# Optimization experiments

Measured on AMD Instinct MI355X. Metric: run time of the kernel, lower is better.

Reference implementation:

```python
import jax, jax.numpy as jnp
import numpy as np

N = 50000   # nodes (cells)
E = 800000  # directed edges
D = 512     # input/output feature dim (genes)
H = D // 64 # bottleneck dim = 8
LN_EPS = 1e-5


def setup_inputs() -> dict:
    key = jax.random.key(0)
    ks = jax.random.split(key, 6)
    x = jax.random.normal(ks[0], (N, D), dtype=jnp.float32)
    edge_index = jax.random.randint(ks[1], (2, E), 0, N, dtype=jnp.int64)
    size_factors = jax.random.uniform(ks[2], (N, 1), dtype=jnp.float32) + 0.5
    s1 = float(1.0 / np.sqrt(D))
    W1 = jax.random.uniform(ks[3], (D, H), jnp.float32, -s1, s1)
    b1 = jnp.zeros((H,), jnp.float32)
    gamma = jnp.ones((H,), jnp.float32)
    beta = jnp.zeros((H,), jnp.float32)
    s2 = float(1.0 / np.sqrt(H))
    W2 = jax.random.uniform(ks[4], (H, D), jnp.float32, -s2, s2)
    b2 = jnp.zeros((D,), jnp.float32)
    return {"x": x, "size_factors": size_factors, "W1": W1, "b1": b1,
            "gamma": gamma, "beta": beta, "W2": W2, "b2": b2,
            "edge_index": edge_index}


def _gcn_conv(x, W, b, src, dst, norm):
    # PyG GCNConv: linear transform, then sym-normalized scatter-add aggregation.
    h = x @ W                                   # [N, out]
    msg = h[src] * norm[:, None]                # [E+N, out] gather + scale
    out = jax.ops.segment_sum(msg, dst, num_segments=N)  # scatter-add
    return out + b


def reference(x, size_factors, W1, b1, gamma, beta, W2, b2, edge_index):
    loops = jnp.arange(N, dtype=edge_index.dtype)
    src = jnp.concatenate([edge_index[0], loops])  # add self-loops
    dst = jnp.concatenate([edge_index[1], loops])
    deg = jax.ops.segment_sum(jnp.ones_like(src, dtype=x.dtype), dst,
                              num_segments=N)       # deg >= 1 via self-loops
    dinv = jax.lax.rsqrt(deg)
    norm = dinv[src] * dinv[dst]                    # [E+N]

    h = _gcn_conv(x, W1, b1, src, dst, norm)        # [N, H]
    mu = jnp.mean(h, axis=-1, keepdims=True)
    var = jnp.var(h, axis=-1, keepdims=True)
    h = (h - mu) * jax.lax.rsqrt(var + LN_EPS) * gamma + beta
    h = jax.nn.relu(h)
    # dropout p=0.0 -> identity
    out = jax.nn.relu(_gcn_conv(h, W2, b2, src, dst, norm))  # [N, D]
    return out * size_factors
```

## Files before the change

kernel.cpp:

```cpp
#include <hip/hip_runtime.h>

#define NN 50000
#define EE 800000
#define DD 512
#define HH 8
#define BA 256
#define CHUNK 3125
#define NBIN 391
#define NBH 512
#define BCAP 2432
#define BPAD 2880
#define GBLK 782
#define NTILE 3125
#define AGBLK 1563

typedef short bf16x8 __attribute__((ext_vector_type(8)));
typedef float f32x4 __attribute__((ext_vector_type(4)));

union U16 { uint4 u; bf16x8 v; unsigned short h[8]; };

__device__ __forceinline__ unsigned short f2bf(float f) {
    union { float f; unsigned int i; } c; c.f = f;
    unsigned int i = c.i;
    i += 0x7fffu + ((i >> 16) & 1u);
    return (unsigned short)(i >> 16);
}

__global__ __launch_bounds__(256) void k_gemm1_hist(const float4* __restrict__ x4,
                                                    const float* __restrict__ W1,
                                                    const int* __restrict__ dst,
                                                    float* __restrict__ t1,
                                                    int* __restrict__ blockhist) {
    __shared__ int smem[4096];
    int t = threadIdx.x;
    if (blockIdx.x >= GBLK) {
        int blk = blockIdx.x - GBLK;
        int* h = smem;
        h[t] = 0; h[t + 256] = 0; __syncthreads();
        int base = blk * CHUNK;
#pragma unroll
        for (int it = 0; it < 13; ++it) {
            int i = it * 256 + t;
            if (i < CHUNK) atomicAdd(&h[dst[base + i] >> 7], 1);
        }
        __syncthreads();
        blockhist[blk * NBH + t] = h[t];
        blockhist[blk * NBH + t + 256] = h[t + 256];
        return;
    }
    unsigned short* sbf = (unsigned short*)smem;
    for (int i = t; i < 16 * 64 * 8; i += 256) {
        int lane = (i >> 3) & 63, j = i & 7;
        int n = lane & 15;
        int k = (i >> 9) * 32 + ((lane >> 4) * 8) + j;
        sbf[i] = (n < HH) ? f2bf(W1[k * HH + n]) : (unsigned short)0;
    }
    __syncthreads();
    int wave = t >> 6, lane = t & 63;
    int tile = blockIdx.x * 4 + wave;
    if (tile >= NTILE) return;
    int node0 = tile * 16;
    int m = lane & 15, q = lane >> 4;
    const float4* xrow = x4 + (size_t)(node0 + m) * (DD / 4) + q * 2;
    const uint4* bfrag = (const uint4*)sbf;
    f32x4 acc = {0.f, 0.f, 0.f, 0.f};

    float4 bufA[8], bufB[8];
#define LOADG(buf, g)                                                      \
    _Pragma("unroll")                                                      \
    for (int s = 0; s < 4; ++s) {                                          \
        buf[2 * s]     = xrow[((g) * 4 + s) * 8];                          \
        buf[2 * s + 1] = xrow[((g) * 4 + s) * 8 + 1];                      \
    }
#define MFMAG(buf, g)                                                      \
    _Pragma("unroll")                                                      \
    for (int s = 0; s < 4; ++s) {                                          \
        U16 a, b;                                                          \
        float4 u0 = buf[2 * s], u1 = buf[2 * s + 1];                       \
        a.h[0] = f2bf(u0.x); a.h[1] = f2bf(u0.y);                          \
        a.h[2] = f2bf(u0.z); a.h[3] = f2bf(u0.w);                          \
        a.h[4] = f2bf(u1.x); a.h[5] = f2bf(u1.y);                          \
        a.h[6] = f2bf(u1.z); a.h[7] = f2bf(u1.w);                          \
        b.u = bfrag[((g) * 4 + s) * 64 + lane];                            \
        acc = __builtin_amdgcn_mfma_f32_16x16x32_bf16(a.v, b.v, acc, 0, 0, 0); \
    }
    LOADG(bufA, 0)
    LOADG(bufB, 1)
    MFMAG(bufA, 0)
    LOADG(bufA, 2)
    MFMAG(bufB, 1)
    LOADG(bufB, 3)
    MFMAG(bufA, 2)
    MFMAG(bufB, 3)
#undef LOADG
#undef MFMAG
    if (m < HH) {
        int base = (node0 + q * 4) * HH + m;
        t1[base]          = acc[0];
        t1[base + HH]     = acc[1];
        t1[base + 2 * HH] = acc[2];
        t1[base + 3 * HH] = acc[3];
    }
}

__global__ __launch_bounds__(256) void k_scan_a(int* __restrict__ blockhist,
                                                int* __restrict__ binTotal) {
    __shared__ int s[256];
    int bin = blockIdx.x, t = threadIdx.x;
    int v = blockhist[t * NBH + bin];
    s[t] = v; __syncthreads();
    for (int off = 1; off < 256; off <<= 1) {
        int x = (t >= off) ? s[t - off] : 0;
        __syncthreads();
        if (t >= off) s[t] += x;
        __syncthreads();
    }
    blockhist[t * NBH + bin] = s[t] - v;
    if (t == 255) binTotal[bin] = s[255];
}

__global__ __launch_bounds__(512) void k_scan_b(const int* __restrict__ binTotal,
                                                int* __restrict__ binBase,
                                                float* __restrict__ t1) {
    __shared__ int s[512];
    int t = threadIdx.x;
    int v = (t < NBIN) ? binTotal[t] : 0;
    s[t] = v; __syncthreads();
    for (int off = 1; off < 512; off <<= 1) {
        int x = (t >= off) ? s[t - off] : 0;
        __syncthreads();
        if (t >= off) s[t] += x;
        __syncthreads();
    }
    if (t < NBIN) binBase[t] = s[t] - v;
    if (t == 511) binBase[NBIN] = s[511];
    if (t < HH) t1[(size_t)NN * HH + t] = 0.f;
}

__global__ __launch_bounds__(256) void k_scatter(const int* __restrict__ eidx,
                                                 const int* __restrict__ blockhist,
                                                 const int* __restrict__ binBase,
                                                 int* __restrict__ bucket) {
    __shared__ int cur[NBH];
    int t = threadIdx.x, blk = blockIdx.x;
    cur[t] = (t < NBIN) ? binBase[t] + blockhist[blk * NBH + t] : 0;
    {
        int i = t + 256;
        cur[i] = (i < NBIN) ? binBase[i] + blockhist[blk * NBH + i] : 0;
    }
    __syncthreads();
    int base = blk * CHUNK;
#pragma unroll
    for (int it = 0; it < 13; ++it) {
        int i = it * 256 + t;
        if (i < CHUNK) {
            int s = eidx[base + i], d = eidx[EE + base + i];
            int pos = atomicAdd(&cur[d >> 7], 1);
            bucket[pos] = (s << 7) | (d & 127);
        }
    }
}

__global__ __launch_bounds__(256) void k_build(const int* __restrict__ bucket,
                                               const int* __restrict__ binBase,
                                               int* __restrict__ beg,
                                               int* __restrict__ endp,
                                               int* __restrict__ adj,
                                               float* __restrict__ dinvA,
                                               float* __restrict__ t1) {
    __shared__ int smem[BCAP + BPAD + 384];
    int t = threadIdx.x;
    int bin = blockIdx.x;
    int n0 = bin << 7;
    int segStart = binBase[bin];
    int count = binBase[bin + 1] - segStart;
    if (count > BCAP) count = BCAP;
    int* lds_in  = smem;
    int* lds_out = smem + BCAP;
    int* cnt     = smem + BCAP + BPAD;
    int* off     = smem + BCAP + BPAD + 128;
    int* cur2    = smem + BCAP + BPAD + 256;
    if (t < 128) cnt[t] = 0;
    __syncthreads();
    for (int i = t; i < count; i += 256) {
        int p = bucket[segStart + i];
        lds_in[i] = p;
        atomicAdd(&cnt[p & 127], 1);
    }
    __syncthreads();
    int pcnt = 0;
    if (t < 128) { pcnt = (cnt[t] + 3) & ~3; off[t] = pcnt; }
    __syncthreads();
    for (int o = 1; o < 128; o <<= 1) {
        int x = (t >= o && t < 128) ? off[t - o] : 0;
        __syncthreads();
        if (t >= o && t < 128) off[t] += x;
        __syncthreads();
    }
    int pbase = ((segStart + 3) & ~3) + bin * 512;
    if (t < 128) {
        int pexcl = off[t] - pcnt;
        cur2[t] = pexcl;
        int n = n0 + t;
        if (n < NN) {
            beg[n]  = pbase + pexcl;
            endp[n] = pbase + pexcl + pcnt;
            float dv = rsqrtf((float)cnt[t] + 1.0f);
            dinvA[n] = dv;
            float4* tp = (float4*)(t1 + (size_t)n * HH);
            float4 a = tp[0], b = tp[1];
            a.x *= dv; a.y *= dv; a.z *= dv; a.w *= dv;
            b.x *= dv; b.y *= dv; b.z *= dv; b.w *= dv;
            tp[0] = a; tp[1] = b;
        }
    }
    __syncthreads();
    int paddedCount = off[127];
    for (int i = t; i < paddedCount; i += 256)
        lds_out[i] = NN;
    __syncthreads();
    for (int i = t; i < count; i += 256) {
        int p = lds_in[i];
        int pos = atomicAdd(&cur2[p & 127], 1);
        lds_out[pos] = p >> 7;
    }
    __syncthreads();
    for (int i = t; i < paddedCount; i += 256)
        adj[pbase + i] = lds_out[i];
}

__global__ __launch_bounds__(256) void k_agg1(const float* __restrict__ t1,
                                              const int* __restrict__ beg,
                                              const int* __restrict__ endp,
                                              const float* __restrict__ dinvA,
                                              const float* __restrict__ b1,
                                              const float* __restrict__ gma,
                                              const float* __restrict__ bta,
                                              const int* __restrict__ adj,
                                              float* __restrict__ h2) {
    if (blockIdx.x == 0 && threadIdx.x < HH)
        h2[(size_t)NN * HH + threadIdx.x] = 0.f;
    int gid = blockIdx.x * 256 + threadIdx.x;
    int n = gid >> 3, f = gid & 7;
    if (n >= NN) return;
    int i = beg[n], e = endp[n];
    float dv = dinvA[n];
    float acc = t1[(size_t)n * HH + f];
    const int4* a4 = (const int4*)adj;
    for (; i + 8 <= e; i += 8) {
        int4 e0 = a4[i >> 2], e1 = a4[(i >> 2) + 1];
        float v0 = t1[(size_t)e0.x * HH + f], v1 = t1[(size_t)e0.y * HH + f];
        float v2 = t1[(size_t)e0.z * HH + f], v3 = t1[(size_t)e0.w * HH + f];
        float v4 = t1[(size_t)e1.x * HH + f], v5 = t1[(size_t)e1.y * HH + f];
        float v6 = t1[(size_t)e1.z * HH + f], v7 = t1[(size_t)e1.w * HH + f];
        acc += ((v0 + v1) + (v2 + v3)) + ((v4 + v5) + (v6 + v7));
    }
    if (i < e) {
        int4 e0 = a4[i >> 2];
        float v0 = t1[(size_t)e0.x * HH + f], v1 = t1[(size_t)e0.y * HH + f];
        float v2 = t1[(size_t)e0.z * HH + f], v3 = t1[(size_t)e0.w * HH + f];
        acc += (v0 + v1) + (v2 + v3);
    }
    acc = acc * dv + b1[f];
    float s = acc;
    s += __shfl_xor(s, 1); s += __shfl_xor(s, 2); s += __shfl_xor(s, 4);
    float mu = s * 0.125f;
    float dx = acc - mu;
    float sq = dx * dx;
    sq += __shfl_xor(sq, 1); sq += __shfl_xor(sq, 2); sq += __shfl_xor(sq, 4);
    float rs = rsqrtf(sq * 0.125f + 1e-5f);
    h2[(size_t)n * HH + f] = fmaxf(dx * rs * gma[f] + bta[f], 0.f) * dv;
}

__global__ __launch_bounds__(256) void k_agg2_gemm2(const float* __restrict__ h2,
                                                    const int* __restrict__ beg,
                                                    const int* __restrict__ endp,
                                                    const float* __restrict__ dinvA,
                                                    const float* __restrict__ W2,
                                                    const float* __restrict__ b2,
                                                    const float* __restrict__ sf,
                                                    const int* __restrict__ adj,
                                                    float* __restrict__ out) {
    __shared__ float sA[32 * 8];
    int tid = threadIdx.x;
    int c = tid & 63, g = tid >> 6, d0 = c * 8;
    float w[8][8];
#pragma unroll
    for (int k = 0; k < 8; ++k) {
        float4 u0 = *(const float4*)(W2 + k * DD + d0);
        float4 u1 = *(const float4*)(W2 + k * DD + d0 + 4);
        w[k][0] = u0.x; w[k][1] = u0.y; w[k][2] = u0.z; w[k][3] = u0.w;
        w[k][4] = u1.x; w[k][5] = u1.y; w[k][6] = u1.z; w[k][7] = u1.w;
    }
    float bb[8];
    {
        float4 u0 = *(const float4*)(b2 + d0);
        float4 u1 = *(const float4*)(b2 + d0 + 4);
        bb[0] = u0.x; bb[1] = u0.y; bb[2] = u0.z; bb[3] = u0.w;
        bb[4] = u1.x; bb[5] = u1.y; bb[6] = u1.z; bb[7] = u1.w;
    }
    int nl = tid >> 3, f = tid & 7;
    int n = blockIdx.x * 32 + nl;
    if (n < NN) {
        int i = beg[n], e = endp[n];
        float dv = dinvA[n];
        float acc = h2[(size_t)n * HH + f];
        const int4* a4 = (const int4*)adj;
        for (; i + 8 <= e; i += 8) {
            int4 e0 = a4[i >> 2], e1 = a4[(i >> 2) + 1];
            float v0 = h2[(size_t)e0.x * HH + f], v1 = h2[(size_t)e0.y * HH + f];
            float v2 = h2[(size_t)e0.z * HH + f], v3 = h2[(size_t)e0.w * HH + f];
            float v4 = h2[(size_t)e1.x * HH + f], v5 = h2[(size_t)e1.y * HH + f];
            float v6 = h2[(size_t)e1.z * HH + f], v7 = h2[(size_t)e1.w * HH + f];
            acc += ((v0 + v1) + (v2 + v3)) + ((v4 + v5) + (v6 + v7));
        }
        if (i < e) {
            int4 e0 = a4[i >> 2];
            float v0 = h2[(size_t)e0.x * HH + f], v1 = h2[(size_t)e0.y * HH + f];
            float v2 = h2[(size_t)e0.z * HH + f], v3 = h2[(size_t)e0.w * HH + f];
            acc += (v0 + v1) + (v2 + v3);
        }
        sA[nl * 8 + f] = acc * dv;
    }
    __syncthreads();
#pragma unroll
    for (int i = 0; i < 8; ++i) {
        int rrow = i * 4 + g;
        int n2 = blockIdx.x * 32 + rrow;
        if (n2 < NN) {
            float a[8];
#pragma unroll
            for (int j = 0; j < 8; ++j) a[j] = sA[rrow * 8 + j];
            float s = sf[n2];
            float acc[8];
#pragma unroll
            for (int j = 0; j < 8; ++j) acc[j] = bb[j];
#pragma unroll
            for (int k = 0; k < 8; ++k)
#pragma unroll
                for (int j = 0; j < 8; ++j) acc[j] += a[k] * w[k][j];
            float4 o0 = make_float4(fmaxf(acc[0], 0.f) * s, fmaxf(acc[1], 0.f) * s,
                                    fmaxf(acc[2], 0.f) * s, fmaxf(acc[3], 0.f) * s);
            float4 o1 = make_float4(fmaxf(acc[4], 0.f) * s, fmaxf(acc[5], 0.f) * s,
                                    fmaxf(acc[6], 0.f) * s, fmaxf(acc[7], 0.f) * s);
            float4* op = (float4*)(out + (size_t)n2 * DD + d0);
            op[0] = o0;
            op[1] = o1;
        }
    }
}

extern "C" void kernel_launch(void* const* d_in, const int* in_sizes, int n_in,
                              void* d_out, int out_size, void* d_ws, size_t ws_size,
                              hipStream_t stream) {
    (void)in_sizes; (void)n_in; (void)out_size; (void)ws_size;
    const float* x   = (const float*)d_in[0];
    const float* sf  = (const float*)d_in[1];
    const float* W1  = (const float*)d_in[2];
    const float* b1  = (const float*)d_in[3];
    const float* gma = (const float*)d_in[4];
    const float* bta = (const float*)d_in[5];
    const float* W2  = (const float*)d_in[6];
    const float* b2  = (const float*)d_in[7];
    const int* eidx  = (const int*)d_in[8];
    float* out = (float*)d_out;

    char* ws = (char*)d_ws;
    int*   blockhist = (int*)(ws + 0);
    int*   binTotal  = (int*)(ws + 0x90000);
    int*   binBase   = (int*)(ws + 0x91000);
    int*   beg       = (int*)(ws + 0x100000);
    int*   endp      = (int*)(ws + 0x140000);
    float* dinvA     = (float*)(ws + 0x200000);
    float* t1        = (float*)(ws + 0x300000);
    float* h2        = (float*)(ws + 0x500000);
    int*   adj       = (int*)(ws + 0x700000);
    int*   bucket    = (int*)(ws + 0xB00000);

    k_gemm1_hist<<<GBLK + BA, 256, 0, stream>>>((const float4*)x, W1, eidx + EE,
                                                t1, blockhist);
    k_scan_a<<<NBIN, 256, 0, stream>>>(blockhist, binTotal);
    k_scan_b<<<1, 512, 0, stream>>>(binTotal, binBase, t1);
    k_scatter<<<BA, 256, 0, stream>>>(eidx, blockhist, binBase, bucket);
    k_build<<<NBIN, 256, 0, stream>>>(bucket, binBase, beg, endp, adj, dinvA, t1);
    k_agg1<<<AGBLK, 256, 0, stream>>>(t1, beg, endp, dinvA, b1, gma, bta, adj, h2);
    k_agg2_gemm2<<<AGBLK, 256, 0, stream>>>(h2, beg, endp, dinvA, W2, b2, sf, adj,
                                            out);
}
```

Measured before the change: 266.1 us.

## Use fixed-capacity bins to drop global scan; split neighbor loops across two lanes

Replaces the second prefix-scan kernel with fixed per-bin capacity slots (bin*CAP in bucket, bin*BSTRIDE in adj), so scatter and build no longer need a global bin base and one launch disappears. The aggregation kernels now assign 16 threads per node instead of 8. Two half-groups each process alternate groups of 4 neighbors and combine with a shuffle, which doubles the thread count to expose more memory-level parallelism. This relies on per-bin counts staying under the fixed capacity, an assumption the code already made by clamping, and it uses more workspace and launches more blocks.

```diff
diff --git a/kernel.cpp b/kernel.cpp
--- a/kernel.cpp
+++ b/kernel.cpp
@@ -8,11 +8,11 @@
 #define CHUNK 3125
 #define NBIN 391
 #define NBH 512
-#define BCAP 2432
-#define BPAD 2880
+#define CAP 2432
+#define BSTRIDE 2816
 #define GBLK 782
 #define NTILE 3125
-#define AGBLK 1563
+#define AGBLK 3125
 
 typedef short bf16x8 __attribute__((ext_vector_type(8)));
 typedef float f32x4 __attribute__((ext_vector_type(4)));
@@ -104,7 +104,8 @@
 }
 
 __global__ __launch_bounds__(256) void k_scan_a(int* __restrict__ blockhist,
-                                                int* __restrict__ binTotal) {
+                                                int* __restrict__ binTotal,
+                                                float* __restrict__ t1) {
     __shared__ int s[256];
     int bin = blockIdx.x, t = threadIdx.x;
     int v = blockhist[t * NBH + bin];
@@ -117,36 +118,18 @@
     }
     blockhist[t * NBH + bin] = s[t] - v;
     if (t == 255) binTotal[bin] = s[255];
-}
-
-__global__ __launch_bounds__(512) void k_scan_b(const int* __restrict__ binTotal,
-                                                int* __restrict__ binBase,
-                                                float* __restrict__ t1) {
-    __shared__ int s[512];
-    int t = threadIdx.x;
-    int v = (t < NBIN) ? binTotal[t] : 0;
-    s[t] = v; __syncthreads();
-    for (int off = 1; off < 512; off <<= 1) {
-        int x = (t >= off) ? s[t - off] : 0;
-        __syncthreads();
-        if (t >= off) s[t] += x;
-        __syncthreads();
-    }
-    if (t < NBIN) binBase[t] = s[t] - v;
-    if (t == 511) binBase[NBIN] = s[511];
-    if (t < HH) t1[(size_t)NN * HH + t] = 0.f;
+    if (bin == 0 && t < HH) t1[(size_t)NN * HH + t] = 0.f;
 }
 
 __global__ __launch_bounds__(256) void k_scatter(const int* __restrict__ eidx,
                                                  const int* __restrict__ blockhist,
-                                                 const int* __restrict__ binBase,
                                                  int* __restrict__ bucket) {
     __shared__ int cur[NBH];
     int t = threadIdx.x, blk = blockIdx.x;
-    cur[t] = (t < NBIN) ? binBase[t] + blockhist[blk * NBH + t] : 0;
+    cur[t] = t * CAP + blockhist[blk * NBH + t];
     {
         int i = t + 256;
-        cur[i] = (i < NBIN) ? binBase[i] + blockhist[blk * NBH + i] : 0;
+        cur[i] = (i < NBIN) ? i * CAP + blockhist[blk * NBH + i] : 0;
     }
     __syncthreads();
     int base = blk * CHUNK;
@@ -162,28 +145,28 @@
 }
 
 __global__ __launch_bounds__(256) void k_build(const int* __restrict__ bucket,
-                                               const int* __restrict__ binBase,
+                                               const int* __restrict__ binTotal,
                                                int* __restrict__ beg,
                                                int* __restrict__ endp,
                                                int* __restrict__ adj,
                                                float* __restrict__ dinvA,
                                                float* __restrict__ t1) {
-    __shared__ int smem[BCAP + BPAD + 384];
+    __shared__ int smem[CAP + BSTRIDE + 384];
     int t = threadIdx.x;
     int bin = blockIdx.x;
     int n0 = bin << 7;
-    int segStart = binBase[bin];
-    int count = binBase[bin + 1] - segStart;
-    if (count > BCAP) count = BCAP;
+    int count = binTotal[bin];
+    if (count > CAP) count = CAP;
+    const int* bsrc = bucket + bin * CAP;
     int* lds_in  = smem;
-    int* lds_out = smem + BCAP;
-    int* cnt     = smem + BCAP + BPAD;
-    int* off     = smem + BCAP + BPAD + 128;
-    int* cur2    = smem + BCAP + BPAD + 256;
+    int* lds_out = smem + CAP;
+    int* cnt     = smem + CAP + BSTRIDE;
+    int* off     = smem + CAP + BSTRIDE + 128;
+    int* cur2    = smem + CAP + BSTRIDE + 256;
     if (t < 128) cnt[t] = 0;
     __syncthreads();
     for (int i = t; i < count; i += 256) {
-        int p = bucket[segStart + i];
+        int p = bsrc[i];
         lds_in[i] = p;
         atomicAdd(&cnt[p & 127], 1);
     }
@@ -197,7 +180,7 @@
         if (t >= o && t < 128) off[t] += x;
         __syncthreads();
     }
-    int pbase = ((segStart + 3) & ~3) + bin * 512;
+    int pbase = bin * BSTRIDE;
     if (t < 128) {
         int pexcl = off[t] - pcnt;
         cur2[t] = pexcl;
@@ -238,29 +221,24 @@
                                               const float* __restrict__ bta,
                                               const int* __restrict__ adj,
                                               float* __restrict__ h2) {
-    if (blockIdx.x == 0 && threadIdx.x < HH)
-        h2[(size_t)NN * HH + threadIdx.x] = 0.f;
-    int gid = blockIdx.x * 256 + threadIdx.x;
-    int n = gid >> 3, f = gid & 7;
+    int t = threadIdx.x;
+    if (blockIdx.x == 0 && t < HH)
+        h2[(size_t)NN * HH + t] = 0.f;
+    int gid = blockIdx.x * 256 + t;
+    int n = gid >> 4, f = t & 7, half = (t >> 3) & 1;
     if (n >= NN) return;
-    int i = beg[n], e = endp[n];
+    int e = endp[n];
+    int i = beg[n] + half * 4;
     float dv = dinvA[n];
-    float acc = t1[(size_t)n * HH + f];
+    float acc = half ? 0.f : t1[(size_t)n * HH + f];
     const int4* a4 = (const int4*)adj;
-    for (; i + 8 <= e; i += 8) {
-        int4 e0 = a4[i >> 2], e1 = a4[(i >> 2) + 1];
-        float v0 = t1[(size_t)e0.x * HH + f], v1 = t1[(size_t)e0.y * HH + f];
-        float v2 = t1[(size_t)e0.z * HH + f], v3 = t1[(size_t)e0.w * HH + f];
-        float v4 = t1[(size_t)e1.x * HH + f], v5 = t1[(size_t)e1.y * HH + f];
-        float v6 = t1[(size_t)e1.z * HH + f], v7 = t1[(size_t)e1.w * HH + f];
-        acc += ((v0 + v1) + (v2 + v3)) + ((v4 + v5) + (v6 + v7));
-    }
-    if (i < e) {
+    for (; i < e; i += 8) {
         int4 e0 = a4[i >> 2];
         float v0 = t1[(size_t)e0.x * HH + f], v1 = t1[(size_t)e0.y * HH + f];
         float v2 = t1[(size_t)e0.z * HH + f], v3 = t1[(size_t)e0.w * HH + f];
         acc += (v0 + v1) + (v2 + v3);
     }
+    acc += __shfl_xor(acc, 8);
     acc = acc * dv + b1[f];
     float s = acc;
     s += __shfl_xor(s, 1); s += __shfl_xor(s, 2); s += __shfl_xor(s, 4);
@@ -269,7 +247,8 @@
     float sq = dx * dx;
     sq += __shfl_xor(sq, 1); sq += __shfl_xor(sq, 2); sq += __shfl_xor(sq, 4);
     float rs = rsqrtf(sq * 0.125f + 1e-5f);
-    h2[(size_t)n * HH + f] = fmaxf(dx * rs * gma[f] + bta[f], 0.f) * dv;
+    if (!half)
+        h2[(size_t)n * HH + f] = fmaxf(dx * rs * gma[f] + bta[f], 0.f) * dv;
 }
 
 __global__ __launch_bounds__(256) void k_agg2_gemm2(const float* __restrict__ h2,
@@ -281,7 +260,7 @@
                                                     const float* __restrict__ sf,
                                                     const int* __restrict__ adj,
                                                     float* __restrict__ out) {
-    __shared__ float sA[32 * 8];
+    __shared__ float sA[16 * 8];
     int tid = threadIdx.x;
     int c = tid & 63, g = tid >> 6, d0 = c * 8;
     float w[8][8];
@@ -299,34 +278,28 @@
         bb[0] = u0.x; bb[1] = u0.y; bb[2] = u0.z; bb[3] = u0.w;
         bb[4] = u1.x; bb[5] = u1.y; bb[6] = u1.z; bb[7] = u1.w;
     }
-    int nl = tid >> 3, f = tid & 7;
-    int n = blockIdx.x * 32 + nl;
+    int nl = tid >> 4, f = tid & 7, half = (tid >> 3) & 1;
+    int n = blockIdx.x * 16 + nl;
     if (n < NN) {
-        int i = beg[n], e = endp[n];
+        int e = endp[n];
+        int i = beg[n] + half * 4;
         float dv = dinvA[n];
-        float acc = h2[(size_t)n * HH + f];
+        float acc = half ? 0.f : h2[(size_t)n * HH + f];
         const int4* a4 = (const int4*)adj;
-        for (; i + 8 <= e; i += 8) {
-            int4 e0 = a4[i >> 2], e1 = a4[(i >> 2) + 1];
-            float v0 = h2[(size_t)e0.x * HH + f], v1 = h2[(size_t)e0.y * HH + f];
-            float v2 = h2[(size_t)e0.z * HH + f], v3 = h2[(size_t)e0.w * HH + f];
-            float v4 = h2[(size_t)e1.x * HH + f], v5 = h2[(size_t)e1.y * HH + f];
-            float v6 = h2[(size_t)e1.z * HH + f], v7 = h2[(size_t)e1.w * HH + f];
-            acc += ((v0 + v1) + (v2 + v3)) + ((v4 + v5) + (v6 + v7));
-        }
-        if (i < e) {
+        for (; i < e; i += 8) {
             int4 e0 = a4[i >> 2];
             float v0 = h2[(size_t)e0.x * HH + f], v1 = h2[(size_t)e0.y * HH + f];
             float v2 = h2[(size_t)e0.z * HH + f], v3 = h2[(size_t)e0.w * HH + f];
             acc += (v0 + v1) + (v2 + v3);
         }
-        sA[nl * 8 + f] = acc * dv;
-    }
-    __syncthreads();
-#pragma unroll
-    for (int i = 0; i < 8; ++i) {
+        acc += __shfl_xor(acc, 8);
+        if (!half) sA[nl * 8 + f] = acc * dv;
+    }
+    __syncthreads();
+#pragma unroll
+    for (int i = 0; i < 4; ++i) {
         int rrow = i * 4 + g;
-        int n2 = blockIdx.x * 32 + rrow;
+        int n2 = blockIdx.x * 16 + rrow;
         if (n2 < NN) {
             float a[8];
 #pragma unroll
@@ -368,21 +341,19 @@
     char* ws = (char*)d_ws;
     int*   blockhist = (int*)(ws + 0);
     int*   binTotal  = (int*)(ws + 0x90000);
-    int*   binBase   = (int*)(ws + 0x91000);
     int*   beg       = (int*)(ws + 0x100000);
     int*   endp      = (int*)(ws + 0x140000);
     float* dinvA     = (float*)(ws + 0x200000);
     float* t1        = (float*)(ws + 0x300000);
     float* h2        = (float*)(ws + 0x500000);
     int*   adj       = (int*)(ws + 0x700000);
-    int*   bucket    = (int*)(ws + 0xB00000);
+    int*   bucket    = (int*)(ws + 0xC00000);
 
     k_gemm1_hist<<<GBLK + BA, 256, 0, stream>>>((const float4*)x, W1, eidx + EE,
                                                 t1, blockhist);
-    k_scan_a<<<NBIN, 256, 0, stream>>>(blockhist, binTotal);
-    k_scan_b<<<1, 512, 0, stream>>>(binTotal, binBase, t1);
-    k_scatter<<<BA, 256, 0, stream>>>(eidx, blockhist, binBase, bucket);
-    k_build<<<NBIN, 256, 0, stream>>>(bucket, binBase, beg, endp, adj, dinvA, t1);
+    k_scan_a<<<NBIN, 256, 0, stream>>>(blockhist, binTotal, t1);
+    k_scatter<<<BA, 256, 0, stream>>>(eidx, blockhist, bucket);
+    k_build<<<NBIN, 256, 0, stream>>>(bucket, binTotal, beg, endp, adj, dinvA, t1);
     k_agg1<<<AGBLK, 256, 0, stream>>>(t1, beg, endp, dinvA, b1, gma, bta, adj, h2);
     k_agg2_gemm2<<<AGBLK, 256, 0, stream>>>(h2, beg, endp, dinvA, W2, b2, sf, adj,
                                             out);
```

Result: no change. 264.1 us (-0.8%).
